# Kernel tuning notes

Measured on AMD Instinct MI355X. Metric: run time of the kernel, lower is better.

The kernel has to match this reference:

```python
import jax, jax.numpy as jnp
import numpy as np

EMBED = 512
HEADS = 8
HIDDEN = 4 * EMBED
EPS = 1e-5


def setup_inputs() -> dict:
    key = jax.random.key(0)
    ks = jax.random.split(key, 12)
    s = lambda fan_in: 1.0 / np.sqrt(fan_in)
    return {
        "x": jax.random.normal(ks[0], (4, 2048, EMBED), dtype=jnp.float32),
        "ln1_g": jnp.ones((EMBED,), jnp.float32),
        "ln1_b": jnp.zeros((EMBED,), jnp.float32),
        "qkv_w": jax.random.uniform(ks[1], (EMBED, 3 * EMBED), jnp.float32, -s(EMBED), s(EMBED)),
        "qkv_b": jax.random.uniform(ks[2], (3 * EMBED,), jnp.float32, -s(EMBED), s(EMBED)),
        "proj_w": jax.random.uniform(ks[3], (EMBED, EMBED), jnp.float32, -s(EMBED), s(EMBED)),
        "proj_b": jax.random.uniform(ks[4], (EMBED,), jnp.float32, -s(EMBED), s(EMBED)),
        "ln2_g": jnp.ones((EMBED,), jnp.float32),
        "ln2_b": jnp.zeros((EMBED,), jnp.float32),
        "fc1_w": jax.random.uniform(ks[5], (EMBED, HIDDEN), jnp.float32, -s(EMBED), s(EMBED)),
        "fc1_b": jax.random.uniform(ks[6], (HIDDEN,), jnp.float32, -s(EMBED), s(EMBED)),
        "fc2_w": jax.random.uniform(ks[7], (HIDDEN, EMBED), jnp.float32, -s(HIDDEN), s(HIDDEN)),
        "fc2_b": jax.random.uniform(ks[8], (EMBED,), jnp.float32, -s(HIDDEN), s(HIDDEN)),
    }


def _layernorm(x, g, b):
    mu = jnp.mean(x, axis=-1, keepdims=True)
    var = jnp.mean(jnp.square(x - mu), axis=-1, keepdims=True)
    return (x - mu) * jax.lax.rsqrt(var + EPS) * g + b


def reference(x, ln1_g, ln1_b, qkv_w, qkv_b, proj_w, proj_b,
              ln2_g, ln2_b, fc1_w, fc1_b, fc2_w, fc2_b):
    B, N, C = x.shape
    H, D = HEADS, C // HEADS
    scale = D ** -0.5

    # --- attention sub-block (pre-LN) ---
    h = _layernorm(x, ln1_g, ln1_b)
    qkv = h @ qkv_w + qkv_b                      # [B,N,3C]
    q, k, v = jnp.split(qkv, 3, axis=-1)
    q = q.reshape(B, N, H, D).transpose(0, 2, 1, 3)  # [B,H,N,D]
    k = k.reshape(B, N, H, D).transpose(0, 2, 1, 3)
    v = v.reshape(B, N, H, D).transpose(0, 2, 1, 3)
    attn = jnp.einsum('bhqd,bhkd->bhqk', q, k) * scale
    attn = jax.nn.softmax(attn, axis=-1)
    o = jnp.einsum('bhqk,bhkd->bhqd', attn, v)
    o = o.transpose(0, 2, 1, 3).reshape(B, N, C)
    x = x + (o @ proj_w + proj_b)

    # --- MLP sub-block (pre-LN, exact GELU) ---
    h = _layernorm(x, ln2_g, ln2_b)
    h = jax.nn.gelu(h @ fc1_w + fc1_b, approximate=False)
    x = x + (h @ fc2_w + fc2_b)
    return x
```

## Files before the change

### kernel.cpp

```cpp
#include <hip/hip_runtime.h>
#include <math.h>


using bf16x8 = __attribute__((ext_vector_type(8))) short;
using f32x4  = __attribute__((ext_vector_type(4))) float;

typedef unsigned short u16;
typedef unsigned int   u32;

__device__ __forceinline__ u16 f2bf(float f) {
    u32 u; __builtin_memcpy(&u, &f, 4);
    u32 r = u + 0x7FFFu + ((u >> 16) & 1u);
    return (u16)(r >> 16);
}
__device__ __forceinline__ u32 fbits(float f) {
    u32 u; __builtin_memcpy(&u, &f, 4); return u;
}
__device__ __forceinline__ float f_from_bits(u32 u) {
    float f; __builtin_memcpy(&f, &u, 4); return f;
}
__device__ __forceinline__ u32 pack_trunc(float lo, float hi) {
    return __builtin_amdgcn_perm(fbits(hi), fbits(lo), 0x07060302u);
}
__device__ __forceinline__ void gload16(const void* g, void* l) {
    __builtin_amdgcn_global_load_lds(
        (const __attribute__((address_space(1))) unsigned int*)g,
        (__attribute__((address_space(3))) unsigned int*)l, 16, 0, 0);
}

__global__ __launch_bounds__(256) void k_pre(
        const float* __restrict__ w0, u16* __restrict__ d0,
        const float* __restrict__ w1, u16* __restrict__ d1,
        const float* __restrict__ w2, u16* __restrict__ d2,
        const float* __restrict__ w3, u16* __restrict__ d3,
        const float* __restrict__ x, const float* __restrict__ g,
        const float* __restrict__ bta, u16* __restrict__ hout) {
    __shared__ float tile[32][33];
    const int bid = blockIdx.x;
    if (bid < 3072) {
        const float* w; u16* dst; int K, N, tb;
        if (bid < 768)       { w = w0; dst = d0; K = 512;  N = 1536; tb = bid; }
        else if (bid < 1024) { w = w1; dst = d1; K = 512;  N = 512;  tb = bid - 768; }
        else if (bid < 2048) { w = w2; dst = d2; K = 512;  N = 2048; tb = bid - 1024; }
        else                 { w = w3; dst = d3; K = 2048; N = 512;  tb = bid - 2048; }
        const int nb = N >> 5;
        const int k0 = (tb / nb) << 5;
        const int n0 = (tb % nb) << 5;
        const int c = threadIdx.x & 31, r = threadIdx.x >> 5;
#pragma unroll
        for (int i = 0; i < 4; i++)
            tile[r + i * 8][c] = w[(size_t)(k0 + r + i * 8) * N + n0 + c];
        __syncthreads();
#pragma unroll
        for (int i = 0; i < 4; i++)
            dst[(size_t)(n0 + r + i * 8) * K + k0 + c] = f2bf(tile[c][r + i * 8]);
    } else {
        const int row  = ((bid - 3072) << 2) + (threadIdx.x >> 6);
        const int lane = threadIdx.x & 63;
        const float* xr = x + (size_t)row * 512 + lane * 8;
        float4 a = *(const float4*)xr;
        float4 c = *(const float4*)(xr + 4);
        float s = a.x + a.y + a.z + a.w + c.x + c.y + c.z + c.w;
        float q = a.x*a.x + a.y*a.y + a.z*a.z + a.w*a.w
                + c.x*c.x + c.y*c.y + c.z*c.z + c.w*c.w;
#pragma unroll
        for (int off = 32; off; off >>= 1) {
            s += __shfl_xor(s, off, 64);
            q += __shfl_xor(q, off, 64);
        }
        const float mean = s * (1.0f / 512.0f);
        const float var  = q * (1.0f / 512.0f) - mean * mean;
        const float rstd = rsqrtf(var + 1e-5f);
        float vv[8] = {a.x, a.y, a.z, a.w, c.x, c.y, c.z, c.w};
#pragma unroll
        for (int j = 0; j < 8; j++) {
            const int col = lane * 8 + j;
            hout[(size_t)row * 512 + col] = f2bf((vv[j] - mean) * rstd * g[col] + bta[col]);
        }
    }
}

__global__ __launch_bounds__(256) void k_ln(const float* __restrict__ x,
                                            const float* __restrict__ g,
                                            const float* __restrict__ bta,
                                            u16* __restrict__ out) {
    const int row  = (blockIdx.x << 2) + (threadIdx.x >> 6);
    const int lane = threadIdx.x & 63;
    const float* xr = x + (size_t)row * 512 + lane * 8;
    float4 a = *(const float4*)xr;
    float4 c = *(const float4*)(xr + 4);
    float s = a.x + a.y + a.z + a.w + c.x + c.y + c.z + c.w;
    float q = a.x*a.x + a.y*a.y + a.z*a.z + a.w*a.w
            + c.x*c.x + c.y*c.y + c.z*c.z + c.w*c.w;
#pragma unroll
    for (int off = 32; off; off >>= 1) {
        s += __shfl_xor(s, off, 64);
        q += __shfl_xor(q, off, 64);
    }
    const float mean = s * (1.0f / 512.0f);
    const float var  = q * (1.0f / 512.0f) - mean * mean;
    const float rstd = rsqrtf(var + 1e-5f);
    float vv[8] = {a.x, a.y, a.z, a.w, c.x, c.y, c.z, c.w};
#pragma unroll
    for (int j = 0; j < 8; j++) {
        const int col = lane * 8 + j;
        out[(size_t)row * 512 + col] = f2bf((vv[j] - mean) * rstd * g[col] + bta[col]);
    }
}

template <int EP, int TN>
__global__ __launch_bounds__(256, 3) void k_gemm(const u16* __restrict__ A,
                                                 const u16* __restrict__ Bt,
                                                 const float* __restrict__ bias,
                                                 const float* __restrict__ res,
                                                 float* __restrict__ outF,
                                                 u16* __restrict__ outB,
                                                 u16* __restrict__ out2,
                                                 int M, int N, int K) {
    constexpr int NT = TN / 32;
    __shared__ u16 As[128 * 64];
    __shared__ u16 Bs[TN * 64];
    const int nb = N / TN;
    const int xg = blockIdx.x & 7, sg = blockIdx.x >> 3;
    const int m0 = ((sg / nb) * 8 + xg) << 7;
    const int n0 = (sg % nb) * TN;
    const int t = threadIdx.x, lane = t & 63, w = t >> 6;
    const int wr = (w >> 1) << 6;
    const int wc = (w & 1) * (TN / 2);
    const int quad = lane >> 4, l15 = lane & 15;
    const int x7 = l15 & 7;

    f32x4 acc[4][NT];
#pragma unroll
    for (int i = 0; i < 4; i++)
#pragma unroll
        for (int j = 0; j < NT; j++) acc[i][j] = (f32x4){0.f, 0.f, 0.f, 0.f};

    const size_t Kb = (size_t)K * 2;
    const char* ga = (const char*)A + (size_t)m0 * Kb;
    const char* gb = (const char*)Bt + (size_t)n0 * Kb;
    const int o0 = t * 16;

    for (int k0 = 0; k0 < K; k0 += 64) {
        const int kb = k0 * 2;
#pragma unroll
        for (int i = 0; i < 4; i++) {
            const int o4 = i * 4096 + o0;
            const int row = o4 >> 7;
            const int lc = ((o4 >> 4) & 7) ^ (row & 7);
            gload16(ga + (size_t)row * Kb + kb + lc * 16, (char*)As + o4);
        }
#pragma unroll
        for (int i = 0; i < TN / 32; i++) {
            const int o4 = i * 4096 + o0;
            const int row = o4 >> 7;
            const int lc = ((o4 >> 4) & 7) ^ (row & 7);
            gload16(gb + (size_t)row * Kb + kb + lc * 16, (char*)Bs + o4);
        }
        __syncthreads();
#pragma unroll
        for (int ks = 0; ks < 2; ks++) {
            const int cidx = ((ks * 4 + quad) ^ x7) * 8;
            bf16x8 af[4], bfr[NT];
#pragma unroll
            for (int i = 0; i < 4; i++)
                af[i] = *(const bf16x8*)(As + (wr + i * 16 + l15) * 64 + cidx);
#pragma unroll
            for (int j = 0; j < NT; j++)
                bfr[j] = *(const bf16x8*)(Bs + (wc + j * 16 + l15) * 64 + cidx);
#pragma unroll
            for (int mt = 0; mt < 4; mt++)
#pragma unroll
                for (int nt = 0; nt < NT; nt++)
                    acc[mt][nt] = __builtin_amdgcn_mfma_f32_16x16x32_bf16(
                        af[mt], bfr[nt], acc[mt][nt], 0, 0, 0);
        }
        __syncthreads();
    }

    const bool vpart = (EP == 3) && (n0 >= 1024);
    const bool qpart = (EP == 3) && (n0 < 512);
#pragma unroll
    for (int mt = 0; mt < 4; mt++)
#pragma unroll
        for (int nt = 0; nt < NT; nt++) {
            const int col = n0 + wc + nt * 16 + l15;
            const float bi = bias[col];
            const int row0 = m0 + wr + mt * 16 + quad * 4;
            if (vpart) {
                const int b = row0 >> 11, key = row0 & 2047;
                const int hd = col - 1024;
                u32 p0 = (u32)f2bf(acc[mt][nt][0] + bi) |
                         ((u32)f2bf(acc[mt][nt][1] + bi) << 16);
                u32 p1 = (u32)f2bf(acc[mt][nt][2] + bi) |
                         ((u32)f2bf(acc[mt][nt][3] + bi) << 16);
                *(uint2*)(out2 + (size_t)(b * 512 + hd) * 2048 + key) = make_uint2(p0, p1);
            } else {
#pragma unroll
                for (int r = 0; r < 4; r++) {
                    const int row = row0 + r;
                    float v = acc[mt][nt][r] + bi;
                    const size_t oi = (size_t)row * N + col;
                    if (EP == 1) {
                        float y = v * (0.79788456f + 0.035677408f * v * v);
                        y = fminf(y, 40.0f);
                        float tE = exp2f(y * 2.88539008f);
                        v = v * tE * __builtin_amdgcn_rcpf(tE + 1.0f);
                    }
                    if (qpart) v *= 0.18033688f;
                    if (EP == 2) outF[oi] = v + res[oi];
                    else         outB[oi] = f2bf(v);
                }
            }
        }
}

__global__ __launch_bounds__(256, 4) void k_attn(const u16* __restrict__ qkv,
                                                 const u16* __restrict__ vt,
                                                 u16* __restrict__ po0,
                                                 u16* __restrict__ po1,
                                                 float* __restrict__ pden) {
    __shared__ u16 smem[16384];
    u16* Ks = smem;
    u16* Vs = smem + 4096;
    u16* Psw = smem + 8192;
    u16* Qs = smem;
    const int bid = blockIdx.x;
    const int h = bid & 7, sg = bid >> 3;
    const int qt = sg & 15, kh = (sg >> 4) & 1, b = sg >> 5;
    const int q0 = qt << 7;
    const int t = threadIdx.x, lane = t & 63, w = t >> 6;
    const int quad = lane >> 4, l15 = lane & 15;
    const int x7 = l15 & 7;

    const char* gq = (const char*)qkv + (size_t)((b << 11) + q0) * 3072 + h * 128;
    const char* gk = (const char*)qkv + (size_t)((b << 11) + (kh << 10)) * 3072 + 1024 + h * 128;
    const char* gv = (const char*)vt + (size_t)((b << 3) + h) * 64 * 4096 + (kh << 10) * 2;

#pragma unroll
    for (int i = 0; i < 4; i++) {
        const int o4 = i * 4096 + t * 16;
        const int row = o4 >> 7;
        const int lc = ((o4 >> 4) & 7) ^ (row & 7);
        gload16(gq + (size_t)row * 3072 + lc * 16, (char*)Qs + o4);
    }
    __syncthreads();

    bf16x8 qf[2][2];
#pragma unroll
    for (int ks = 0; ks < 2; ks++) {
        const int cidx = ((ks * 4 + quad) ^ x7) * 8;
#pragma unroll
        for (int nt = 0; nt < 2; nt++)
            qf[ks][nt] = *(const bf16x8*)(Qs + (w * 32 + nt * 16 + l15) * 64 + cidx);
    }
    __syncthreads();

    f32x4 accO[4][2];
    float denp[2] = {0.f, 0.f};
#pragma unroll
    for (int mt = 0; mt < 4; mt++)
#pragma unroll
        for (int nt = 0; nt < 2; nt++) accO[mt][nt] = (f32x4){0.f, 0.f, 0.f, 0.f};

    for (int kt = 0; kt < 16; kt++) {
        const int kk = kt << 6;
#pragma unroll
        for (int i = 0; i < 2; i++) {
            const int o4 = i * 4096 + t * 16;
            const int row = o4 >> 7;
            const int lc = ((o4 >> 4) & 7) ^ (row & 7);
            gload16(gk + (size_t)(kk + row) * 3072 + lc * 16, (char*)Ks + o4);
            gload16(gv + (size_t)row * 4096 + kk * 2 + lc * 16, (char*)Vs + o4);
        }
        __syncthreads();

        f32x4 s[4][2];
#pragma unroll
        for (int mt = 0; mt < 4; mt++)
#pragma unroll
            for (int nt = 0; nt < 2; nt++) s[mt][nt] = (f32x4){0.f, 0.f, 0.f, 0.f};
#pragma unroll
        for (int ks = 0; ks < 2; ks++) {
            const int cidx = ((ks * 4 + quad) ^ x7) * 8;
            bf16x8 kf[4];
#pragma unroll
            for (int mt = 0; mt < 4; mt++)
                kf[mt] = *(const bf16x8*)(Ks + (mt * 16 + l15) * 64 + cidx);
#pragma unroll
            for (int mt = 0; mt < 4; mt++)
#pragma unroll
                for (int nt = 0; nt < 2; nt++)
                    s[mt][nt] = __builtin_amdgcn_mfma_f32_16x16x32_bf16(
                        kf[mt], qf[ks][nt], s[mt][nt], 0, 0, 0);
        }

#pragma unroll
        for (int mt = 0; mt < 4; mt++)
#pragma unroll
            for (int nt = 0; nt < 2; nt++) {
                const float p0 = exp2f(s[mt][nt][0]);
                const float p1 = exp2f(s[mt][nt][1]);
                const float p2 = exp2f(s[mt][nt][2]);
                const float p3 = exp2f(s[mt][nt][3]);
                denp[nt] += (p0 + p1) + (p2 + p3);
                const u32 d0 = pack_trunc(p0, p1);
                const u32 d1 = pack_trunc(p2, p3);
                const int pidx = (nt * 16 + l15) * 64 +
                                 (((2 * mt + (quad >> 1)) ^ x7) << 3) + (quad & 1) * 4;
                *(uint2*)(&Psw[w * 2048 + pidx]) = make_uint2(d0, d1);
            }

#pragma unroll
        for (int ks = 0; ks < 2; ks++) {
            const int cidx = ((ks * 4 + quad) ^ x7) * 8;
            bf16x8 vf[4], pf[2];
#pragma unroll
            for (int mt = 0; mt < 4; mt++)
                vf[mt] = *(const bf16x8*)(Vs + (mt * 16 + l15) * 64 + cidx);
#pragma unroll
            for (int nt = 0; nt < 2; nt++)
                pf[nt] = *(const bf16x8*)(Psw + w * 2048 + (nt * 16 + l15) * 64 + cidx);
#pragma unroll
            for (int mt = 0; mt < 4; mt++)
#pragma unroll
                for (int nt = 0; nt < 2; nt++)
                    accO[mt][nt] = __builtin_amdgcn_mfma_f32_16x16x32_bf16(
                        vf[mt], pf[nt], accO[mt][nt], 0, 0, 0);
        }
        __syncthreads();
    }

    u16* po = kh ? po1 : po0;
#pragma unroll
    for (int nt = 0; nt < 2; nt++) {
        float dn = denp[nt];
        dn += __shfl_xor(dn, 16, 64);
        dn += __shfl_xor(dn, 32, 64);
        if (quad == 0)
            pden[(size_t)(((kh << 5) + (b << 3) + h) << 11) + q0 + w * 32 + nt * 16 + l15] = dn;
#pragma unroll
        for (int mt = 0; mt < 4; mt++) {
            const int qg = q0 + w * 32 + nt * 16 + l15;
            const u32 p0 = (u32)f2bf(accO[mt][nt][0]) | ((u32)f2bf(accO[mt][nt][1]) << 16);
            const u32 p1 = (u32)f2bf(accO[mt][nt][2]) | ((u32)f2bf(accO[mt][nt][3]) << 16);
            *(uint2*)(po + (size_t)((b << 11) + qg) * 512 + h * 64 + mt * 16 + quad * 4) =
                make_uint2(p0, p1);
        }
    }
}

__global__ __launch_bounds__(256) void k_combine(u16* __restrict__ po0,
                                                 const u16* __restrict__ po1,
                                                 const float* __restrict__ pden) {
    const int idx8 = (blockIdx.x * 256 + threadIdx.x) * 8;
    const int row = idx8 >> 9, col = idx8 & 511;
    const int h = col >> 6, q = row & 2047, b = row >> 11;
    const size_t di = (size_t)(((b << 3) + h) << 11) + q;
    const float den = pden[di] + pden[di + (32 << 11)];
    const float r = __builtin_amdgcn_rcpf(den);
    uint4 a = *(const uint4*)(po0 + idx8);
    uint4 c = *(const uint4*)(po1 + idx8);
    u32 av[4] = {a.x, a.y, a.z, a.w}, cv[4] = {c.x, c.y, c.z, c.w}, ov[4];
#pragma unroll
    for (int i = 0; i < 4; i++) {
        const float lo = (f_from_bits(av[i] << 16) + f_from_bits(cv[i] << 16)) * r;
        const float hi = (f_from_bits(av[i] & 0xFFFF0000u) +
                          f_from_bits(cv[i] & 0xFFFF0000u)) * r;
        ov[i] = (u32)f2bf(lo) | ((u32)f2bf(hi) << 16);
    }
    *(uint4*)(po0 + idx8) = make_uint4(ov[0], ov[1], ov[2], ov[3]);
}

extern "C" void kernel_launch(void* const* d_in, const int* in_sizes, int n_in,
                              void* d_out, int out_size, void* d_ws, size_t ws_size,
                              hipStream_t stream) {
    const float* x      = (const float*)d_in[0];
    const float* ln1_g  = (const float*)d_in[1];
    const float* ln1_b  = (const float*)d_in[2];
    const float* qkv_w  = (const float*)d_in[3];
    const float* qkv_b  = (const float*)d_in[4];
    const float* proj_w = (const float*)d_in[5];
    const float* proj_b = (const float*)d_in[6];
    const float* ln2_g  = (const float*)d_in[7];
    const float* ln2_b  = (const float*)d_in[8];
    const float* fc1_w  = (const float*)d_in[9];
    const float* fc1_b  = (const float*)d_in[10];
    const float* fc2_w  = (const float*)d_in[11];
    const float* fc2_b  = (const float*)d_in[12];
    float* out = (float*)d_out;
    char* ws = (char*)d_ws;

    u16*   qkv_wT = (u16*)(ws + 0);
    u16*   proj_wT= (u16*)(ws + 1572864);
    u16*   fc1_wT = (u16*)(ws + 2097152);
    u16*   fc2_wT = (u16*)(ws + 4194304);
    u16*   h      = (u16*)(ws + 6291456);
    float* pden   = (float*)(ws + 6291456);
    u16*   qkv    = (u16*)(ws + 14680064);
    u16*   vt     = (u16*)(ws + 39845888);
    u16*   o      = (u16*)(ws + 48234496);
    u16*   po1    = (u16*)(ws + 56623104);
    float* x1     = (float*)(ws + 56623104);
    u16*   f1     = (u16*)(ws + 14680064);
    u16*   h2     = h;

    k_pre<<<5120, 256, 0, stream>>>(qkv_w, qkv_wT, proj_w, proj_wT,
                                    fc1_w, fc1_wT, fc2_w, fc2_wT,
                                    x, ln1_g, ln1_b, h);
    k_gemm<3,128><<<(8192/128)*(1536/128), 256, 0, stream>>>(
        h, qkv_wT, qkv_b, nullptr, nullptr, qkv, vt, 8192, 1536, 512);
    k_attn<<<1024, 256, 0, stream>>>(qkv, vt, o, po1, pden);
    k_combine<<<2048, 256, 0, stream>>>(o, po1, pden);
    k_gemm<2,64><<<(8192/128)*(512/64), 256, 0, stream>>>(
        o, proj_wT, proj_b, x, x1, nullptr, nullptr, 8192, 512, 512);
    k_ln<<<2048, 256, 0, stream>>>(x1, ln2_g, ln2_b, h2);
    k_gemm<1,128><<<(8192/128)*(2048/128), 256, 0, stream>>>(
        h2, fc1_wT, fc1_b, nullptr, nullptr, f1, nullptr, 8192, 2048, 512);
    k_gemm<2,64><<<(8192/128)*(512/64), 256, 0, stream>>>(
        f1, fc2_wT, fc2_b, x1, out, nullptr, nullptr, 8192, 512, 2048);
}
```

Before: 259.4 us.

## Double-buffer K/V tiles in attention kernel and load Q directly into registers

The attention kernel now prefetches the next K/V tile into a second LDS buffer while computing on the current one, needing only one barrier per iteration instead of two. Q fragments are read straight from global memory into registers rather than staged through LDS. The P staging buffer is halved by processing one query sub-tile at a time, and exp2f is swapped for the hardware exp2 intrinsic. LDS use per block rises to 40KB, which may limit occupancy at four blocks per CU, and the uncoalesced direct Q loads could cost some bandwidth.

```diff
diff --git a/kernel.cpp b/kernel.cpp
--- a/kernel.cpp
+++ b/kernel.cpp
@@ -220,11 +220,7 @@
                                                  u16* __restrict__ po0,
                                                  u16* __restrict__ po1,
                                                  float* __restrict__ pden) {
-    __shared__ u16 smem[16384];
-    u16* Ks = smem;
-    u16* Vs = smem + 4096;
-    u16* Psw = smem + 8192;
-    u16* Qs = smem;
+    __shared__ u16 smem[20480];
     const int bid = blockIdx.x;
     const int h = bid & 7, sg = bid >> 3;
     const int qt = sg & 15, kh = (sg >> 4) & 1, b = sg >> 5;
@@ -233,28 +229,28 @@
     const int quad = lane >> 4, l15 = lane & 15;
     const int x7 = l15 & 7;
 
-    const char* gq = (const char*)qkv + (size_t)((b << 11) + q0) * 3072 + h * 128;
+    char* sb = (char*)smem;
     const char* gk = (const char*)qkv + (size_t)((b << 11) + (kh << 10)) * 3072 + 1024 + h * 128;
     const char* gv = (const char*)vt + (size_t)((b << 3) + h) * 64 * 4096 + (kh << 10) * 2;
 
 #pragma unroll
-    for (int i = 0; i < 4; i++) {
+    for (int i = 0; i < 2; i++) {
         const int o4 = i * 4096 + t * 16;
         const int row = o4 >> 7;
         const int lc = ((o4 >> 4) & 7) ^ (row & 7);
-        gload16(gq + (size_t)row * 3072 + lc * 16, (char*)Qs + o4);
-    }
-    __syncthreads();
+        gload16(gk + (size_t)row * 3072 + lc * 16, sb + o4);
+        gload16(gv + (size_t)row * 4096 + lc * 16, sb + 8192 + o4);
+    }
 
     bf16x8 qf[2][2];
-#pragma unroll
-    for (int ks = 0; ks < 2; ks++) {
-        const int cidx = ((ks * 4 + quad) ^ x7) * 8;
-#pragma unroll
-        for (int nt = 0; nt < 2; nt++)
-            qf[ks][nt] = *(const bf16x8*)(Qs + (w * 32 + nt * 16 + l15) * 64 + cidx);
-    }
-    __syncthreads();
+    {
+        const u16* gqp = qkv + (size_t)((b << 11) + q0 + w * 32 + l15) * 1536 + h * 64;
+#pragma unroll
+        for (int ks = 0; ks < 2; ks++)
+#pragma unroll
+            for (int nt = 0; nt < 2; nt++)
+                qf[ks][nt] = *(const bf16x8*)(gqp + (size_t)(nt * 16) * 1536 + (ks * 4 + quad) * 8);
+    }
 
     f32x4 accO[4][2];
     float denp[2] = {0.f, 0.f};
@@ -263,17 +259,25 @@
 #pragma unroll
         for (int nt = 0; nt < 2; nt++) accO[mt][nt] = (f32x4){0.f, 0.f, 0.f, 0.f};
 
+    u16* Pw = smem + 16384 + w * 1024;
+
     for (int kt = 0; kt < 16; kt++) {
-        const int kk = kt << 6;
-#pragma unroll
-        for (int i = 0; i < 2; i++) {
-            const int o4 = i * 4096 + t * 16;
-            const int row = o4 >> 7;
-            const int lc = ((o4 >> 4) & 7) ^ (row & 7);
-            gload16(gk + (size_t)(kk + row) * 3072 + lc * 16, (char*)Ks + o4);
-            gload16(gv + (size_t)row * 4096 + kk * 2 + lc * 16, (char*)Vs + o4);
-        }
+        const int cur = kt & 1;
         __syncthreads();
+        if (kt < 15) {
+            const int kk2 = (kt + 1) << 6;
+            char* db = sb + (cur ^ 1) * 16384;
+#pragma unroll
+            for (int i = 0; i < 2; i++) {
+                const int o4 = i * 4096 + t * 16;
+                const int row = o4 >> 7;
+                const int lc = ((o4 >> 4) & 7) ^ (row & 7);
+                gload16(gk + (size_t)(kk2 + row) * 3072 + lc * 16, db + o4);
+                gload16(gv + (size_t)row * 4096 + (size_t)kk2 * 2 + lc * 16, db + 8192 + o4);
+            }
+        }
+        const u16* Ksc = smem + cur * 8192;
+        const u16* Vsc = Ksc + 4096;
 
         f32x4 s[4][2];
 #pragma unroll
@@ -286,7 +290,7 @@
             bf16x8 kf[4];
 #pragma unroll
             for (int mt = 0; mt < 4; mt++)
-                kf[mt] = *(const bf16x8*)(Ks + (mt * 16 + l15) * 64 + cidx);
+                kf[mt] = *(const bf16x8*)(Ksc + (mt * 16 + l15) * 64 + cidx);
 #pragma unroll
             for (int mt = 0; mt < 4; mt++)
 #pragma unroll
@@ -296,39 +300,34 @@
         }
 
 #pragma unroll
-        for (int mt = 0; mt < 4; mt++)
-#pragma unroll
-            for (int nt = 0; nt < 2; nt++) {
-                const float p0 = exp2f(s[mt][nt][0]);
-                const float p1 = exp2f(s[mt][nt][1]);
-                const float p2 = exp2f(s[mt][nt][2]);
-                const float p3 = exp2f(s[mt][nt][3]);
+        for (int nt = 0; nt < 2; nt++) {
+#pragma unroll
+            for (int mt = 0; mt < 4; mt++) {
+                const float p0 = __builtin_amdgcn_exp2f(s[mt][nt][0]);
+                const float p1 = __builtin_amdgcn_exp2f(s[mt][nt][1]);
+                const float p2 = __builtin_amdgcn_exp2f(s[mt][nt][2]);
+                const float p3 = __builtin_amdgcn_exp2f(s[mt][nt][3]);
                 denp[nt] += (p0 + p1) + (p2 + p3);
                 const u32 d0 = pack_trunc(p0, p1);
                 const u32 d1 = pack_trunc(p2, p3);
-                const int pidx = (nt * 16 + l15) * 64 +
+                const int pidx = l15 * 64 +
                                  (((2 * mt + (quad >> 1)) ^ x7) << 3) + (quad & 1) * 4;
-                *(uint2*)(&Psw[w * 2048 + pidx]) = make_uint2(d0, d1);
+                *(uint2*)(&Pw[pidx]) = make_uint2(d0, d1);
             }
-
-#pragma unroll
-        for (int ks = 0; ks < 2; ks++) {
-            const int cidx = ((ks * 4 + quad) ^ x7) * 8;
-            bf16x8 vf[4], pf[2];
-#pragma unroll
-            for (int mt = 0; mt < 4; mt++)
-                vf[mt] = *(const bf16x8*)(Vs + (mt * 16 + l15) * 64 + cidx);
-#pragma unroll
-            for (int nt = 0; nt < 2; nt++)
-                pf[nt] = *(const bf16x8*)(Psw + w * 2048 + (nt * 16 + l15) * 64 + cidx);
-#pragma unroll
-            for (int mt = 0; mt < 4; mt++)
-#pragma unroll
-                for (int nt = 0; nt < 2; nt++)
+#pragma unroll
+            for (int ks = 0; ks < 2; ks++) {
+                const int cidx = ((ks * 4 + quad) ^ x7) * 8;
+                bf16x8 vf[4];
+#pragma unroll
+                for (int mt = 0; mt < 4; mt++)
+                    vf[mt] = *(const bf16x8*)(Vsc + (mt * 16 + l15) * 64 + cidx);
+                const bf16x8 pf = *(const bf16x8*)(Pw + l15 * 64 + cidx);
+#pragma unroll
+                for (int mt = 0; mt < 4; mt++)
                     accO[mt][nt] = __builtin_amdgcn_mfma_f32_16x16x32_bf16(
-                        vf[mt], pf[nt], accO[mt][nt], 0, 0, 0);
-        }
-        __syncthreads();
+                        vf[mt], pf, accO[mt][nt], 0, 0, 0);
+            }
+        }
     }
 
     u16* po = kh ? po1 : po0;
```

Result: faster. 248.1 us (-4.3%).
